# Kernel tuning notes

Measured on AMD Instinct MI355X. Metric: run time of the kernel, lower is better.

The kernel has to match this reference:

```python
import jax, jax.numpy as jnp
import numpy as np

N_HEAD = 16

def setup_inputs() -> dict:
    key = jax.random.key(0)
    k1, k2, k3, k4, k5 = jax.random.split(key, 5)
    B, T, C = 2, 2048, 1024
    scale = 1.0 / np.sqrt(C)
    return {
        "x": jax.random.normal(k1, (B, T, C), dtype=jnp.float32),
        "Wqkv": jax.random.normal(k2, (C, 3 * C), dtype=jnp.float32) * scale,
        "bqkv": jax.random.normal(k3, (3 * C,), dtype=jnp.float32) * 0.02,
        "Wproj": jax.random.normal(k4, (C, C), dtype=jnp.float32) * scale,
        "bproj": jax.random.normal(k5, (C,), dtype=jnp.float32) * 0.02,
    }

def reference(x, Wqkv, bqkv, Wproj, bproj):
    B, T, C = x.shape
    H = N_HEAD
    D = C // H
    # qkv projection, split last dim as (3, H, D): first C cols = q, etc.
    qkv = (x @ Wqkv + bqkv).reshape(B, T, 3, H, D)
    q, k, v = qkv[:, :, 0], qkv[:, :, 1], qkv[:, :, 2]  # (B, T, H, D)
    att = jnp.einsum("bqhd,bkhd->bhqk", q, k) * (1.0 / np.sqrt(D))
    causal = jnp.tril(jnp.ones((T, T), dtype=bool))
    att = jnp.where(causal, att, -jnp.inf)
    att = jax.nn.softmax(att, axis=-1)
    y = jnp.einsum("bhqk,bkhd->bqhd", att, v).reshape(B, T, C)
    return y @ Wproj + bproj
```

## Files before the change

### kernel.cpp

```cpp
#include <hip/hip_runtime.h>
#include <hip/hip_bf16.h>
#include <stdint.h>

typedef unsigned short u16;
typedef __attribute__((ext_vector_type(8))) short bf16x8;
typedef __attribute__((ext_vector_type(4))) float f32x4;

#define MFMA16(a,b,c) __builtin_amdgcn_mfma_f32_16x16x32_bf16((a),(b),(c),0,0,0)

__device__ __forceinline__ u16 f2bf(float f) {
    union { float f; uint32_t u; } v; v.f = f;
    return (u16)((v.u + 0x7FFFu + ((v.u >> 16) & 1u)) >> 16);
}

__global__ void k_convert(const float* __restrict__ in, u16* __restrict__ out) {
    int i = (blockIdx.x * 256 + threadIdx.x) * 4;
    f32x4 v = *(const f32x4*)(in + i);
    uint64_t p = (uint64_t)f2bf(v[0]) | ((uint64_t)f2bf(v[1]) << 16)
               | ((uint64_t)f2bf(v[2]) << 32) | ((uint64_t)f2bf(v[3]) << 48);
    *(uint64_t*)(out + i) = p;
}

__global__ void k_transpose_convert(const float* __restrict__ W, u16* __restrict__ WT,
                                    int R, int NC) {
    int id = blockIdx.x * 256 + threadIdx.x;
    int n = id % NC, kc = id / NC;
    bf16x8 o;
#pragma unroll
    for (int i = 0; i < 8; ++i)
        o[i] = (short)f2bf(W[(size_t)(kc * 8 + i) * NC + n]);
    *(bf16x8*)(WT + (size_t)n * R + kc * 8) = o;
}

template<int NREP, int MODE>
__device__ __forceinline__ void gemm_body(
    const u16* __restrict__ A, const u16* __restrict__ Bt,
    const float* __restrict__ bias,
    u16* __restrict__ outQKV, float* __restrict__ outF,
    int M, int N, int tileId, int K)
{
    constexpr int BN = 32 * NREP;
    constexpr int WN = 16 * NREP;
    constexpr int BSLOTS = NREP / 2;
    __shared__ __align__(16) u16 As[3][128 * 32];
    __shared__ __align__(16) u16 Bs[3][BN * 32];
    const int tid = threadIdx.x;
    const int nbx = N / BN;
    const int bm = tileId / nbx, bn = tileId % nbx;
    const int m0 = bm << 7, n0 = bn * BN;
    const int l = tid & 63, w = tid >> 6;
    const int wr = w >> 1, wc = w & 1;
    const int kl = l >> 4, lr = l & 15;

    const u16* Ag = A + (size_t)m0 * K;
    const u16* Bg = Bt + (size_t)n0 * K;

    int a_src[2], a_dst[2];
#pragma unroll
    for (int s = 0; s < 2; ++s) {
        int cb = w * 128 + s * 64;
        int c = cb + l;
        int r = c >> 2, kc = c & 3;
        a_src[s] = r * K + ((kc ^ ((r >> 1) & 3)) << 3);
        a_dst[s] = cb << 3;
    }
    int b_src[BSLOTS], b_dst[BSLOTS];
#pragma unroll
    for (int s = 0; s < BSLOTS; ++s) {
        int cb = (w * BSLOTS + s) * 64;
        int c = cb + l;
        int r = c >> 2, kc = c & 3;
        b_src[s] = r * K + ((kc ^ ((r >> 1) & 3)) << 3);
        b_dst[s] = cb << 3;
    }

    int ra[4], rb[NREP];
#pragma unroll
    for (int m = 0; m < 4; ++m) {
        int row = wr * 64 + m * 16 + lr;
        ra[m] = row * 32 + (((kl ^ (row >> 1)) & 3) << 3);
    }
#pragma unroll
    for (int n = 0; n < NREP; ++n) {
        int row = wc * WN + n * 16 + lr;
        rb[n] = row * 32 + (((kl ^ (row >> 1)) & 3) << 3);
    }

    f32x4 acc[4][NREP] = {};

    auto STAGE = [&](int buf, int koff) {
#pragma unroll
        for (int s = 0; s < 2; ++s)
            __builtin_amdgcn_global_load_lds(Ag + a_src[s] + koff,
                                             &As[buf][a_dst[s]], 16, 0, 0);
#pragma unroll
        for (int s = 0; s < BSLOTS; ++s)
            __builtin_amdgcn_global_load_lds(Bg + b_src[s] + koff,
                                             &Bs[buf][b_dst[s]], 16, 0, 0);
    };

    STAGE(0, 0);
    STAGE(1, 32);
    if constexpr (NREP == 4) asm volatile("s_waitcnt vmcnt(4)" ::: "memory");
    else                     asm volatile("s_waitcnt vmcnt(3)" ::: "memory");
    __builtin_amdgcn_s_barrier();
    __builtin_amdgcn_sched_barrier(0);

    const int nK = K >> 5;
    int rd = 0;
    for (int ks = 0; ks < nK; ++ks) {
        const bool st = (ks + 2 < nK);
        if (st) {
            int sb = rd + 2; if (sb >= 3) sb -= 3;
            STAGE(sb, (ks + 2) << 5);
        }
        bf16x8 af[4], bfr[NREP];
#pragma unroll
        for (int m = 0; m < 4; ++m) af[m] = *(const bf16x8*)&As[rd][ra[m]];
#pragma unroll
        for (int n = 0; n < NREP; ++n) bfr[n] = *(const bf16x8*)&Bs[rd][rb[n]];
#pragma unroll
        for (int m = 0; m < 4; ++m)
#pragma unroll
            for (int n = 0; n < NREP; ++n)
                acc[m][n] = MFMA16(af[m], bfr[n], acc[m][n]);
        if (ks + 1 < nK) {
            if (st) {
                if constexpr (NREP == 4) asm volatile("s_waitcnt vmcnt(4)" ::: "memory");
                else                     asm volatile("s_waitcnt vmcnt(3)" ::: "memory");
            } else {
                asm volatile("s_waitcnt vmcnt(0)" ::: "memory");
            }
            __builtin_amdgcn_s_barrier();
            __builtin_amdgcn_sched_barrier(0);
        }
        rd = (rd == 2) ? 0 : rd + 1;
    }

    if (MODE == 0) {
#pragma unroll
        for (int n = 0; n < NREP; ++n) {
            int gn = n0 + wc * WN + n * 16 + lr;
            float bv = bias[gn];
            int s = gn >> 10, hd = gn & 1023;
            int hh = hd >> 6, dd = hd & 63;
            if (s == 2) {
                size_t vb = (size_t)2 * 4194304 + (size_t)hh * 131072
                          + (size_t)dd * 2048;
#pragma unroll
                for (int m = 0; m < 4; ++m) {
                    int gm = m0 + wr * 64 + m * 16 + kl * 4;
                    int bb = gm >> 11, tt = gm & 2047;
                    uint64_t p = (uint64_t)f2bf(acc[m][n][0] + bv)
                               | ((uint64_t)f2bf(acc[m][n][1] + bv) << 16)
                               | ((uint64_t)f2bf(acc[m][n][2] + bv) << 32)
                               | ((uint64_t)f2bf(acc[m][n][3] + bv) << 48);
                    *(uint64_t*)(outQKV + vb + (size_t)bb * 2097152 + tt) = p;
                }
            } else {
                float mult = (s == 0) ? 0.125f : 1.0f;
                size_t base = (size_t)s * 4194304 + (size_t)hh * 131072 + dd;
#pragma unroll
                for (int m = 0; m < 4; ++m)
#pragma unroll
                    for (int j = 0; j < 4; ++j) {
                        int gm = m0 + wr * 64 + m * 16 + kl * 4 + j;
                        int bb = gm >> 11, tt = gm & 2047;
                        float val = (acc[m][n][j] + bv) * mult;
                        outQKV[base + (size_t)bb * 2097152 + (size_t)tt * 64] = f2bf(val);
                    }
            }
        }
    } else {
#pragma unroll
        for (int n = 0; n < NREP; ++n) {
            int gn = n0 + wc * WN + n * 16 + lr;
            float bv = bias[gn];
#pragma unroll
            for (int m = 0; m < 4; ++m)
#pragma unroll
                for (int j = 0; j < 4; ++j) {
                    int gm = m0 + wr * 64 + m * 16 + kl * 4 + j;
                    outF[(size_t)gm * N + gn] = acc[m][n][j] + bv;
                }
        }
    }
}

__global__ __launch_bounds__(256, 3) void k_gemm_qkv(
    const u16* __restrict__ A, const u16* __restrict__ Bt,
    const float* __restrict__ bias, u16* __restrict__ outQKV,
    int M, int N, int K)
{
    int tile = (blockIdx.x & 7) * (gridDim.x >> 3) + (blockIdx.x >> 3);
    gemm_body<4, 0>(A, Bt, bias, outQKV, nullptr, M, N, tile, K);
}

__global__ __launch_bounds__(256, 3) void k_gemm_proj(
    const u16* __restrict__ A, const u16* __restrict__ Bt,
    const float* __restrict__ bias, float* __restrict__ outF,
    int M, int N, int K)
{
    int tile = (blockIdx.x & 7) * (gridDim.x >> 3) + (blockIdx.x >> 3);
    gemm_body<2, 1>(A, Bt, bias, nullptr, outF, M, N, tile, K);
}

__global__ __launch_bounds__(256, 4) void k_attn(
    const u16* __restrict__ Qg, const u16* __restrict__ Kg,
    const u16* __restrict__ Vtg, u16* __restrict__ Yg)
{
    const int bid = blockIdx.x;
    const int bh = bid & 31;
    const int qt = 31 - (bid >> 5);
    const int b = bh >> 4, h = bh & 15;
    const int q0 = qt << 6;
    const int tid = threadIdx.x, l = tid & 63, w = tid >> 6;
    const int kl = l >> 4, lr = l & 15;

    __shared__ __align__(16) u16 Qs[64 * 64];
    __shared__ __align__(16) u16 Ks[64 * 64];
    __shared__ __align__(16) u16 Vs[64 * 64];
    __shared__ __align__(16) u16 Ps[4][16 * 72];

    const u16* Qb = Qg + (size_t)bh * 131072;
    const u16* Kb = Kg + (size_t)bh * 131072;
    const u16* Vb = Vtg + (size_t)bh * 131072;

    const int rr = tid >> 3, ch = tid & 7;
    {
        bf16x8 a = *(const bf16x8*)(Qb + (size_t)(q0 + rr) * 64 + ch * 8);
        bf16x8 c = *(const bf16x8*)(Qb + (size_t)(q0 + rr + 32) * 64 + ch * 8);
        *(bf16x8*)&Qs[rr * 64 + ((ch ^ (rr & 7)) << 3)] = a;
        *(bf16x8*)&Qs[(rr + 32) * 64 + ((ch ^ (rr & 7)) << 3)] = c;
    }
    __syncthreads();
    bf16x8 qa[2];
#pragma unroll
    for (int kk = 0; kk < 2; ++kk) {
        int row = w * 16 + lr;
        qa[kk] = *(const bf16x8*)&Qs[row * 64 + (((kk * 4 + kl) ^ (row & 7)) << 3)];
    }

    f32x4 oacc[4] = {};
    float lsum[4] = {0.f, 0.f, 0.f, 0.f};

    bf16x8 kv0 = *(const bf16x8*)(Kb + (size_t)rr * 64 + ch * 8);
    bf16x8 kv1 = *(const bf16x8*)(Kb + (size_t)(rr + 32) * 64 + ch * 8);
    bf16x8 vv0 = *(const bf16x8*)(Vb + (size_t)rr * 2048 + ch * 8);
    bf16x8 vv1 = *(const bf16x8*)(Vb + (size_t)(rr + 32) * 2048 + ch * 8);

    for (int kt = 0; kt <= qt; ++kt) {
        const int k0 = kt << 6;
        __syncthreads();
        *(bf16x8*)&Ks[rr * 64 + ((ch ^ (rr & 7)) << 3)] = kv0;
        *(bf16x8*)&Ks[(rr + 32) * 64 + ((ch ^ (rr & 7)) << 3)] = kv1;
        *(bf16x8*)&Vs[rr * 64 + ((ch ^ (rr & 7)) << 3)] = vv0;
        *(bf16x8*)&Vs[(rr + 32) * 64 + ((ch ^ (rr & 7)) << 3)] = vv1;
        __syncthreads();
        if (kt < qt) {
            const int k0n = k0 + 64;
            kv0 = *(const bf16x8*)(Kb + (size_t)(k0n + rr) * 64 + ch * 8);
            kv1 = *(const bf16x8*)(Kb + (size_t)(k0n + rr + 32) * 64 + ch * 8);
            vv0 = *(const bf16x8*)(Vb + (size_t)rr * 2048 + k0n + ch * 8);
            vv1 = *(const bf16x8*)(Vb + (size_t)(rr + 32) * 2048 + k0n + ch * 8);
        }

        f32x4 s[4];
#pragma unroll
        for (int nb = 0; nb < 4; ++nb) {
            f32x4 a = {};
            int key = nb * 16 + lr;
#pragma unroll
            for (int kk = 0; kk < 2; ++kk) {
                bf16x8 kb = *(const bf16x8*)&Ks[key * 64 + (((kk * 4 + kl) ^ (key & 7)) << 3)];
                a = MFMA16(qa[kk], kb, a);
            }
            s[nb] = a;
        }
        if (kt == qt) {
#pragma unroll
            for (int nb = 0; nb < 4; ++nb) {
                int key = k0 + nb * 16 + lr;
#pragma unroll
                for (int j = 0; j < 4; ++j) {
                    int q = q0 + w * 16 + kl * 4 + j;
                    if (key > q) s[nb][j] = -__builtin_inff();
                }
            }
        }
#pragma unroll
        for (int j = 0; j < 4; ++j) {
            float acc4 = 0.f;
#pragma unroll
            for (int nb = 0; nb < 4; ++nb) {
                float p = __expf(s[nb][j]);
                s[nb][j] = p;
                acc4 += p;
            }
            lsum[j] += acc4;
        }
#pragma unroll
        for (int nb = 0; nb < 4; ++nb)
#pragma unroll
            for (int j = 0; j < 4; ++j)
                Ps[w][(kl * 4 + j) * 72 + nb * 16 + lr] = f2bf(s[nb][j]);
        bf16x8 pa[2];
#pragma unroll
        for (int kk = 0; kk < 2; ++kk)
            pa[kk] = *(const bf16x8*)&Ps[w][lr * 72 + kk * 32 + kl * 8];
#pragma unroll
        for (int db = 0; db < 4; ++db) {
            int d = db * 16 + lr;
#pragma unroll
            for (int kk = 0; kk < 2; ++kk) {
                bf16x8 vb = *(const bf16x8*)&Vs[d * 64 + (((kk * 4 + kl) ^ (d & 7)) << 3)];
                oacc[db] = MFMA16(pa[kk], vb, oacc[db]);
            }
        }
    }
#pragma unroll
    for (int j = 0; j < 4; ++j) {
#pragma unroll
        for (int off = 1; off < 16; off <<= 1) lsum[j] += __shfl_xor(lsum[j], off);
        lsum[j] = 1.f / lsum[j];
    }
#pragma unroll
    for (int db = 0; db < 4; ++db)
#pragma unroll
        for (int j = 0; j < 4; ++j) {
            int q = q0 + w * 16 + kl * 4 + j;
            int col = h * 64 + db * 16 + lr;
            Yg[(size_t)(b * 2048 + q) * 1024 + col] = f2bf(oacc[db][j] * lsum[j]);
        }
}

extern "C" void kernel_launch(void* const* d_in, const int* in_sizes, int n_in,
                              void* d_out, int out_size, void* d_ws, size_t ws_size,
                              hipStream_t stream) {
    const float* x     = (const float*)d_in[0];
    const float* Wqkv  = (const float*)d_in[1];
    const float* bqkv  = (const float*)d_in[2];
    const float* Wproj = (const float*)d_in[3];
    const float* bproj = (const float*)d_in[4];
    float* out = (float*)d_out;

    char* ws = (char*)d_ws;
    u16* xb     = (u16*)(ws);
    u16* WqkvT  = (u16*)(ws + 8388608);
    u16* WprojT = (u16*)(ws + 14680064);
    u16* qkv    = (u16*)(ws + 16777216);
    u16* Vt   = qkv + 2 * 4194304;
    u16* Yatt = xb;

    k_convert<<<4096, 256, 0, stream>>>(x, xb);
    k_transpose_convert<<<1536, 256, 0, stream>>>(Wqkv, WqkvT, 1024, 3072);
    k_transpose_convert<<<512, 256, 0, stream>>>(Wproj, WprojT, 1024, 1024);
    k_gemm_qkv<<<768, 256, 0, stream>>>(xb, WqkvT, bqkv, qkv,
                                        4096, 3072, 1024);
    k_attn<<<1024, 256, 0, stream>>>(qkv, qkv + 4194304, Vt, Yatt);
    k_gemm_proj<<<512, 256, 0, stream>>>(Yatt, WprojT, bproj, out,
                                         4096, 1024, 1024);
}
```

Baseline: 113.5 us.

## Transpose QK^T MFMA output, fold log2e into Q scale, pack P stores

Swaps the MFMA operands so each lane holds scores for one query row across 4 consecutive keys. The P tile can then be written to LDS with packed 64-bit stores using the hardware bf16 pack-convert instruction, and each lane keeps a single row sum that needs only two cross-lane shuffles. It also folds log2(e) into the Q pre-scale so the softmax uses exp2 directly. The aim is to cut LDS scalar stores, software bf16 rounding and shuffle reductions in the attention inner loop. In exchange, the final normalization needs extra shuffles to redistribute the row sums, and the pack instruction's rounding may differ slightly from the software round-to-nearest-even.

```diff
diff --git a/kernel.cpp b/kernel.cpp
--- a/kernel.cpp
+++ b/kernel.cpp
@@ -1,6 +1,7 @@
 #include <hip/hip_runtime.h>
 #include <hip/hip_bf16.h>
 #include <stdint.h>
+#include <math.h>
 
 typedef unsigned short u16;
 typedef __attribute__((ext_vector_type(8))) short bf16x8;
@@ -11,6 +12,12 @@
 __device__ __forceinline__ u16 f2bf(float f) {
     union { float f; uint32_t u; } v; v.f = f;
     return (u16)((v.u + 0x7FFFu + ((v.u >> 16) & 1u)) >> 16);
+}
+
+__device__ __forceinline__ uint32_t cvt_pk_bf16(float lo, float hi) {
+    uint32_t r;
+    asm("v_cvt_pk_bf16_f32 %0, %1, %2" : "=v"(r) : "v"(lo), "v"(hi));
+    return r;
 }
 
 __global__ void k_convert(const float* __restrict__ in, u16* __restrict__ out) {
@@ -158,7 +165,7 @@
                     *(uint64_t*)(outQKV + vb + (size_t)bb * 2097152 + tt) = p;
                 }
             } else {
-                float mult = (s == 0) ? 0.125f : 1.0f;
+                float mult = (s == 0) ? 0.18033688f : 1.0f;
                 size_t base = (size_t)s * 4194304 + (size_t)hh * 131072 + dd;
 #pragma unroll
                 for (int m = 0; m < 4; ++m)
@@ -242,7 +249,7 @@
     }
 
     f32x4 oacc[4] = {};
-    float lsum[4] = {0.f, 0.f, 0.f, 0.f};
+    float lsum = 0.f;
 
     bf16x8 kv0 = *(const bf16x8*)(Kb + (size_t)rr * 64 + ch * 8);
     bf16x8 kv1 = *(const bf16x8*)(Kb + (size_t)(rr + 32) * 64 + ch * 8);
@@ -273,37 +280,34 @@
 #pragma unroll
             for (int kk = 0; kk < 2; ++kk) {
                 bf16x8 kb = *(const bf16x8*)&Ks[key * 64 + (((kk * 4 + kl) ^ (key & 7)) << 3)];
-                a = MFMA16(qa[kk], kb, a);
+                a = MFMA16(kb, qa[kk], a);
             }
             s[nb] = a;
         }
         if (kt == qt) {
+            int q = q0 + w * 16 + lr;
 #pragma unroll
             for (int nb = 0; nb < 4; ++nb) {
-                int key = k0 + nb * 16 + lr;
-#pragma unroll
-                for (int j = 0; j < 4; ++j) {
-                    int q = q0 + w * 16 + kl * 4 + j;
-                    if (key > q) s[nb][j] = -__builtin_inff();
-                }
-            }
-        }
-#pragma unroll
-        for (int j = 0; j < 4; ++j) {
-            float acc4 = 0.f;
-#pragma unroll
-            for (int nb = 0; nb < 4; ++nb) {
-                float p = __expf(s[nb][j]);
-                s[nb][j] = p;
-                acc4 += p;
-            }
-            lsum[j] += acc4;
-        }
-#pragma unroll
-        for (int nb = 0; nb < 4; ++nb)
-#pragma unroll
-            for (int j = 0; j < 4; ++j)
-                Ps[w][(kl * 4 + j) * 72 + nb * 16 + lr] = f2bf(s[nb][j]);
+                int keyb = k0 + nb * 16 + kl * 4;
+#pragma unroll
+                for (int j = 0; j < 4; ++j)
+                    if (keyb + j > q) s[nb][j] = -__builtin_inff();
+            }
+        }
+        float acc16 = 0.f;
+#pragma unroll
+        for (int nb = 0; nb < 4; ++nb) {
+#pragma unroll
+            for (int j = 0; j < 4; ++j) {
+                s[nb][j] = exp2f(s[nb][j]);
+                acc16 += s[nb][j];
+            }
+            uint64_t pk = (uint64_t)cvt_pk_bf16(s[nb][0], s[nb][1])
+                        | ((uint64_t)cvt_pk_bf16(s[nb][2], s[nb][3]) << 32);
+            *(uint64_t*)&Ps[w][lr * 72 + nb * 16 + kl * 4] = pk;
+        }
+        lsum += acc16;
+
         bf16x8 pa[2];
 #pragma unroll
         for (int kk = 0; kk < 2; ++kk)
@@ -318,19 +322,19 @@
             }
         }
     }
-#pragma unroll
-    for (int j = 0; j < 4; ++j) {
-#pragma unroll
-        for (int off = 1; off < 16; off <<= 1) lsum[j] += __shfl_xor(lsum[j], off);
-        lsum[j] = 1.f / lsum[j];
-    }
+    lsum += __shfl_xor(lsum, 16);
+    lsum += __shfl_xor(lsum, 32);
+    float linv[4];
+#pragma unroll
+    for (int j = 0; j < 4; ++j)
+        linv[j] = 1.f / __shfl(lsum, kl * 4 + j);
 #pragma unroll
     for (int db = 0; db < 4; ++db)
 #pragma unroll
         for (int j = 0; j < 4; ++j) {
             int q = q0 + w * 16 + kl * 4 + j;
             int col = h * 64 + db * 16 + lr;
-            Yg[(size_t)(b * 2048 + q) * 1024 + col] = f2bf(oacc[db][j] * lsum[j]);
+            Yg[(size_t)(b * 2048 + q) * 1024 + col] = f2bf(oacc[db][j] * linv[j]);
         }
 }
 
```

New measurement: 111.9 us. About the same (-1.4%).
